# Kernel optimization log

Measured on AMD Instinct MI355X. Metric: run time of the kernel, lower is better.

## Reference

```python
import jax, jax.numpy as jnp
import numpy as np

C0, C1 = 8, 4            # scalar / vector channels (type_in = type_out = [8,4])
K = 5                    # p-space kernel size
G = 8                    # number of gaussian radial basis functions
EPS = 1e-6               # zero-length epsilon
R_MAX = 5.5              # max |p_off - q_diff| ~ sqrt(3)*2 + 2


def _levi_civita():
    e = np.zeros((3, 3, 3), np.float32)
    e[0, 1, 2] = e[1, 2, 0] = e[2, 0, 1] = 1.0
    e[0, 2, 1] = e[2, 1, 0] = e[1, 0, 2] = -1.0
    return jnp.asarray(e)


def setup_inputs() -> dict:
    key = jax.random.key(0)
    ks = jax.random.split(key, 10)
    N, Q, P = 1, 16, 8
    dim = C0 + 3 * C1
    x = jax.random.normal(ks[0], (N, dim, Q, P, P, P), jnp.float32)

    def qschema(k):
        q = jax.random.normal(k, (Q, 3), jnp.float32)
        return q / jnp.max(jnp.linalg.norm(q, axis=-1))  # normalize lengths to <= 1

    q_in, q_out = qschema(ks[1]), qschema(ks[2])
    s = 0.1
    w_ss = s * jax.random.normal(ks[3], (C0, C0, G), jnp.float32)
    w_vs = s * jax.random.normal(ks[4], (C1, C0, G), jnp.float32)
    w_sv = s * jax.random.normal(ks[5], (C0, C1, G), jnp.float32)
    w_vv0 = s * jax.random.normal(ks[6], (C1, C1, G), jnp.float32)
    w_vv1 = s * jax.random.normal(ks[7], (C1, C1, G), jnp.float32)
    bias = s * jax.random.normal(ks[8], (C0,), jnp.float32)
    return dict(x=x, q_in=q_in, q_out=q_out, w_ss=w_ss, w_vs=w_vs, w_sv=w_sv,
                w_vv0=w_vv0, w_vv1=w_vv1, bias=bias)


def reference(x, q_in, q_out, w_ss, w_vs, w_sv, w_vv0, w_vv1, bias):
    N, dim_in, Qi = x.shape[0], x.shape[1], x.shape[2]
    Qo = q_out.shape[0]
    K3 = K ** 3
    # p-space tap offsets (voxel units, zyx) of the 5x5x5 kernel
    offs = jnp.arange(K, dtype=x.dtype) - (K - 1) / 2.0
    oz, oy, ox = jnp.meshgrid(offs, offs, offs, indexing='ij')
    p_off = jnp.stack([oz, oy, ox], -1).reshape(-1, 3)                       # (K3,3)
    # pq_diff geometry: v = p_offset - (q_out - q_in)
    v = p_off[None, None] - (q_out[:, None, None] - q_in[None, :, None])     # (Qo,Qi,K3,3)
    r = jnp.linalg.norm(v, axis=-1)                                          # (Qo,Qi,K3)
    u = jnp.where(r[..., None] > EPS, v / jnp.maximum(r, EPS)[..., None], 0.0)
    # gaussian radial basis on |v|
    centers = jnp.linspace(0.0, R_MAX, G).astype(x.dtype)
    sigma = R_MAX / (G - 1)
    R = jnp.exp(-0.5 * ((r[..., None] - centers) / sigma) ** 2)              # (Qo,Qi,K3,G)
    RY = R[..., None] * u[..., None, :]                                      # (Qo,Qi,K3,G,3) radial x Y_1
    eye3 = jnp.eye(3, dtype=x.dtype)
    eps3 = _levi_civita().astype(x.dtype)
    # CG paths (l_in,l_out,l_f): axes a=out ch, c=in ch, p=Qo, q=Qi, k=tap, g=radial, m/n/i/j=vec comps
    K_ss = jnp.einsum('acg,pqkg->apcqk', w_ss, R)                            # (0,0,0)
    K_vs = jnp.einsum('acg,pqkgm->ampcqk', w_vs, RY)                         # (0,1,1)
    K_sv = jnp.einsum('acg,pqkgm->apcmqk', w_sv, RY)                         # (1,0,1)
    K_vv = (jnp.einsum('acg,pqkg,mn->ampcnqk', w_vv0, R, eye3)               # (1,1,0) identity
            + 0.7071067811865476 *
            jnp.einsum('acg,pqkgm,imj->aipcjqk', w_vv1, RY, eps3))           # (1,1,1) cross prod
    top = jnp.concatenate([K_ss, K_sv.reshape(C0, Qo, 3 * C1, Qi, K3)], axis=2)
    bot = jnp.concatenate([K_vs.reshape(3 * C1, Qo, C0, Qi, K3),
                           K_vv.reshape(3 * C1, Qo, 3 * C1, Qi, K3)], axis=2)
    kern = jnp.concatenate([top, bot], axis=0)                               # (dim_out,Qo,dim_in,Qi,K3)
    dim_out = C0 + 3 * C1
    kern = kern.reshape(dim_out * Qo, dim_in * Qi, K, K, K)
    xr = x.reshape(N, dim_in * Qi, *x.shape[3:])
    out = jax.lax.conv_general_dilated(
        xr, kern, window_strides=(1, 1, 1), padding='SAME',
        dimension_numbers=('NCDHW', 'OIDHW', 'NCDHW'))
    out = out.reshape(N, dim_out, Qo, *x.shape[3:])
    b_full = jnp.concatenate([bias, jnp.zeros(3 * C1, bias.dtype)])
    return out + b_full.reshape(1, dim_out, 1, 1, 1, 1)
```

## Files before the change

kernel.cpp:

```cpp
#include <hip/hip_runtime.h>
#include <hip/hip_bf16.h>
#include <math.h>

#define C0 8
#define C1 4
#define NCH 20
#define NQ 16
#define K3 125
#define G 8
#define RMAX 5.5f
#define EPSL 1e-6f

#define KD1 2048
#define PHI_N 1048576
#define XTP_N 552960
#define W2_N 20480
#define KD2 640
#define E2C_B 10485760

#define LDS_A 18432
#define LDS_B 27648

using f32x4 = __attribute__((ext_vector_type(4))) float;
using s16x8 = __attribute__((ext_vector_type(8))) short;

__device__ __forceinline__ float epsf(int i, int m, int j) {
    if (i == m || m == j || i == j) return 0.f;
    return (m == (i + 1) % 3) ? 1.f : -1.f;
}

__global__ __launch_bounds__(256) void prep_kernel(
    const float* __restrict__ x,
    const float* __restrict__ q_in, const float* __restrict__ q_out,
    const float* __restrict__ w_ss, const float* __restrict__ w_vs,
    const float* __restrict__ w_sv, const float* __restrict__ w_vv0,
    const float* __restrict__ w_vv1,
    __hip_bfloat16* __restrict__ phi, __hip_bfloat16* __restrict__ xtp,
    __hip_bfloat16* __restrict__ w2)
{
    int gid = blockIdx.x * 256 + threadIdx.x;
    if (gid < PHI_N) {
        int col = gid & (KD1 - 1); int m = gid >> 11;
        int t = col >> 4, q = col & 15;
        int p = m >> 5,  b = m & 31;
        int g = b >> 2,  mi = b & 3;
        float val = 0.f;
        if (t < K3) {
            int tz = t / 25, ty = (t / 5) % 5, tx = t % 5;
            float vz = (float)(tz - 2) - (q_out[p*3+0] - q_in[q*3+0]);
            float vy = (float)(ty - 2) - (q_out[p*3+1] - q_in[q*3+1]);
            float vx = (float)(tx - 2) - (q_out[p*3+2] - q_in[q*3+2]);
            float r  = sqrtf(vz*vz + vy*vy + vx*vx);
            float inv = (r > EPSL) ? (1.0f / r) : 0.0f;
            const float sigma = RMAX / (float)(G - 1);
            float d = (r - (RMAX * (float)g / (float)(G - 1))) / sigma;
            float Rg = expf(-0.5f * d * d);
            float u = (mi == 1) ? vz*inv : ((mi == 2) ? vy*inv : vx*inv);
            val = (mi == 0) ? Rg : Rg * u;
        }
        phi[gid] = __float2bfloat16(val);
    } else if (gid < PHI_N + XTP_N) {
        int g2 = gid - PHI_N;
        int q = g2 & 15; int r = g2 >> 4;
        int ax = r % 12; r /= 12;
        int ay = r % 12; r /= 12;
        int az = r % 12; int c = r / 12;
        int iz = az - 2, iy = ay - 2, ix = ax - 2;
        bool valid = ((unsigned)iz < 8u) & ((unsigned)iy < 8u) & ((unsigned)ix < 8u);
        float v = valid ? x[((c * NQ + q) << 9) + (iz << 6) + (iy << 3) + ix] : 0.f;
        xtp[g2] = __float2bfloat16(v);
    } else {
        int id = gid - (PHI_N + XTP_N);
        int b = id & 31; int r = id >> 5;
        int c = r % NCH; int o = r / NCH;
        int g = b >> 2,  mi = b & 3;
        float val = 0.f;
        if (o < NCH) {
            if (o < C0) {
                if (c < C0) { if (mi == 0) val = w_ss[(o * C0 + c) * G + g]; }
                else { int cv = (c - C0) / 3, j = (c - C0) % 3;
                       if (mi == 1 + j) val = w_sv[(o * C1 + cv) * G + g]; }
            } else {
                int ov = (o - C0) / 3, i = (o - C0) % 3;
                if (c < C0) { if (mi == 1 + i) val = w_vs[(ov * C0 + c) * G + g]; }
                else {
                    int cv = (c - C0) / 3, j = (c - C0) % 3;
                    if (mi == 0) { if (i == j) val = w_vv0[(ov * C1 + cv) * G + g]; }
                    else val = 0.7071067811865476f * w_vv1[(ov * C1 + cv) * G + g]
                               * epsf(i, mi - 1, j);
                }
            }
        }
        w2[id] = __float2bfloat16(val);
    }
}

__global__ __launch_bounds__(256, 3) void gemm1_kernel(
    const char* __restrict__ phi_b, const char* __restrict__ xtp_b,
    char* __restrict__ E2_b)
{
    __shared__ __align__(16) char lds[LDS_A + LDS_B];

    int tid = threadIdx.x;
    int wave = tid >> 6, lane = tid & 63;
    int row = lane & 15, quad = lane >> 4;
    int wi = wave >> 1, wj = wave & 1;

    int bi = blockIdx.x;
    int kc = bi / 320;
    int r  = bi - kc * 320;
    int pg = r / 80;
    int r2 = r - pg * 80;
    int c  = r2 >> 2;
    int zq = r2 & 3;

    {
        const char* src = xtp_b + c * 55296 + zq * 9216;
        for (int i = tid; i < 1728; i += 256)
            *(s16x8*)(lds + LDS_A + i * 16) = *(const s16x8*)(src + i * 16);
    }

    const char* abase = phi_b + (size_t)(pg * 128) * 4096 + kc * 2048;
    int srow[4], skp[4];
    #pragma unroll
    for (int i = 0; i < 4; ++i) { int s = tid + i * 256; srow[i] = s >> 3; skp[i] = s & 7; }
    s16x8 areg[4];
    #pragma unroll
    for (int i = 0; i < 4; ++i)
        areg[i] = *(const s16x8*)(abase + srow[i] * 4096 + skp[i] * 16);

    int bpre[4];
    #pragma unroll
    for (int nt = 0; nt < 4; ++nt) {
        int zl = wj * 64 + nt * 16 + row;
        int zz = zl >> 6, zy = (zl >> 3) & 7, zx = zl & 7;
        bpre[nt] = LDS_A + (zz * 144 + zy * 12 + zx) * 32 + (quad & 1) * 16;
    }
    int hi = quad >> 1;

    f32x4 acc[4][4];
    #pragma unroll
    for (int i = 0; i < 4; ++i)
        #pragma unroll
        for (int j = 0; j < 4; ++j) acc[i][j] = (f32x4){0.f, 0.f, 0.f, 0.f};

    for (int j = 0; j < 16; ++j) {
        int toff[4];
        #pragma unroll
        for (int tt = 0; tt < 4; ++tt) {
            int t = kc * 64 + j * 4 + tt; if (t > 124) t = 124;
            int tz = t / 25, trm = t - tz * 25;
            int ty = trm / 5, tx = trm - ty * 5;
            toff[tt] = (tz * 144 + ty * 12 + tx) * 32;
        }
        #pragma unroll
        for (int i = 0; i < 4; ++i)
            *(s16x8*)(lds + srow[i] * 144 + skp[i] * 16) = areg[i];
        __syncthreads();
        if (j < 15) {
            #pragma unroll
            for (int i = 0; i < 4; ++i)
                areg[i] = *(const s16x8*)(abase + srow[i] * 4096 + (j + 1) * 128 + skp[i] * 16);
        }
        #pragma unroll
        for (int st = 0; st < 2; ++st) {
            s16x8 af[4], bf[4];
            #pragma unroll
            for (int mt = 0; mt < 4; ++mt)
                af[mt] = *(const s16x8*)(lds + (wi * 64 + mt * 16 + row) * 144
                                             + (st * 4 + quad) * 16);
            int tsel = toff[st * 2 + hi];
            #pragma unroll
            for (int nt = 0; nt < 4; ++nt)
                bf[nt] = *(const s16x8*)(lds + bpre[nt] + tsel);
            #pragma unroll
            for (int mt = 0; mt < 4; ++mt)
                #pragma unroll
                for (int nt = 0; nt < 4; ++nt)
                    acc[mt][nt] = __builtin_amdgcn_mfma_f32_16x16x32_bf16(
                        af[mt], bf[nt], acc[mt][nt], 0, 0, 0);
        }
        __syncthreads();
    }

    int wbase = wave * 8704;
    #pragma unroll
    for (int mt = 0; mt < 4; ++mt) {
        #pragma unroll
        for (int nt = 0; nt < 4; ++nt) {
            int zl = nt * 16 + row;
            union { unsigned long long u; __hip_bfloat16 h[4]; } pk;
            pk.h[0] = __float2bfloat16(acc[mt][nt][0]);
            pk.h[1] = __float2bfloat16(acc[mt][nt][1]);
            pk.h[2] = __float2bfloat16(acc[mt][nt][2]);
            pk.h[3] = __float2bfloat16(acc[mt][nt][3]);
            *(unsigned long long*)(lds + wbase + zl * 136 + (mt * 16 + quad * 4) * 2) = pk.u;
        }
    }
    char* Ek = E2_b + (size_t)kc * E2C_B;
    int pbase = pg * 4 + wi * 2;
    #pragma unroll
    for (int it = 0; it < 8; ++it) {
        int item = lane + it * 64;
        int piece = item & 3;
        int zl = (item >> 2) & 63;
        int h  = item >> 8;
        s16x8 v = *(const s16x8*)(lds + wbase + zl * 136 + h * 64 + piece * 16);
        int p = pbase + h;
        int z = zq * 128 + wj * 64 + zl;
        *(s16x8*)(Ek + ((size_t)((p * NCH + c) << 9) + z) * 64 + piece * 16) = v;
    }
}

__global__ __launch_bounds__(128) void gemm2_kernel(
    const char* __restrict__ w2_b, const char* __restrict__ E2_b,
    const float* __restrict__ bias, float* __restrict__ out)
{
    int tid = threadIdx.x;
    int wave = tid >> 6, lane = tid & 63;
    int row = lane & 15, quad = lane >> 4;
    int bi = blockIdx.x;
    int p  = bi >> 4;
    int zb = bi & 15;
    int z  = zb * 32 + wave * 16 + row;

    const char* bbase = E2_b + (size_t)p * 655360 + (size_t)z * 64 + quad * 16;

    f32x4 acc[2];
    acc[0] = (f32x4){0.f, 0.f, 0.f, 0.f};
    acc[1] = (f32x4){0.f, 0.f, 0.f, 0.f};

    for (int kc = 0; kc < 2; ++kc) {
        const char* bk = bbase + (size_t)kc * E2C_B;
        #pragma unroll 5
        for (int cc = 0; cc < NCH; ++cc) {
            s16x8 a0 = *(const s16x8*)(w2_b + (row)      * 1280 + cc * 64 + quad * 16);
            s16x8 a1 = *(const s16x8*)(w2_b + (16 + row) * 1280 + cc * 64 + quad * 16);
            s16x8 b  = *(const s16x8*)(bk + (size_t)cc * 32768);
            acc[0] = __builtin_amdgcn_mfma_f32_16x16x32_bf16(a0, b, acc[0], 0, 0, 0);
            acc[1] = __builtin_amdgcn_mfma_f32_16x16x32_bf16(a1, b, acc[1], 0, 0, 0);
        }
    }

    #pragma unroll
    for (int mt = 0; mt < 2; ++mt)
        #pragma unroll
        for (int ri = 0; ri < 4; ++ri) {
            int o = mt * 16 + quad * 4 + ri;
            if (o < NCH)
                out[((o * NQ + p) << 9) + z] = acc[mt][ri] + ((o < C0) ? bias[o] : 0.f);
        }
}

extern "C" void kernel_launch(void* const* d_in, const int* in_sizes, int n_in,
                              void* d_out, int out_size, void* d_ws, size_t ws_size,
                              hipStream_t stream) {
    const float* x     = (const float*)d_in[0];
    const float* q_in  = (const float*)d_in[1];
    const float* q_out = (const float*)d_in[2];
    const float* w_ss  = (const float*)d_in[3];
    const float* w_vs  = (const float*)d_in[4];
    const float* w_sv  = (const float*)d_in[5];
    const float* w_vv0 = (const float*)d_in[6];
    const float* w_vv1 = (const float*)d_in[7];
    const float* bias  = (const float*)d_in[8];
    float* out = (float*)d_out;

    char* ws = (char*)d_ws;
    __hip_bfloat16* phi = (__hip_bfloat16*)(ws + 0);
    __hip_bfloat16* xtp = (__hip_bfloat16*)(ws + 2097152);
    __hip_bfloat16* w2  = (__hip_bfloat16*)(ws + 3203072);
    char*           E2  = (char*)(ws + 3244032);

    const int PREP_N = PHI_N + XTP_N + W2_N;
    hipLaunchKernelGGL(prep_kernel, dim3(PREP_N / 256), dim3(256), 0, stream,
                       x, q_in, q_out, w_ss, w_vs, w_sv, w_vv0, w_vv1, phi, xtp, w2);
    hipLaunchKernelGGL(gemm1_kernel, dim3(640), dim3(256), 0, stream,
                       (const char*)phi, (const char*)xtp, E2);
    hipLaunchKernelGGL(gemm2_kernel, dim3(256), dim3(128), 0, stream,
                       (const char*)w2, (const char*)E2, bias, out);
}
```

Measured before the change: 117.3 us.

## Split gemm2 reduction across blocks with atomic accumulation and bias prefill

Splits the gemm2 reduction over the two kc chunks and two channel halves into separate blocks, growing the grid from 256 to 1024 blocks to occupy more CUs. Partial sums are combined with float atomicAdd into the output. The output is first filled with the bias (or zero) by an extra section of prep_kernel. This adds atomic traffic, makes the summation order nondeterministic, and adds an output initialization pass.

```diff
diff --git a/kernel.cpp b/kernel.cpp
--- a/kernel.cpp
+++ b/kernel.cpp
@@ -15,7 +15,7 @@
 #define PHI_N 1048576
 #define XTP_N 552960
 #define W2_N 20480
-#define KD2 640
+#define OUT_N 163840
 #define E2C_B 10485760
 
 #define LDS_A 18432
@@ -34,9 +34,9 @@
     const float* __restrict__ q_in, const float* __restrict__ q_out,
     const float* __restrict__ w_ss, const float* __restrict__ w_vs,
     const float* __restrict__ w_sv, const float* __restrict__ w_vv0,
-    const float* __restrict__ w_vv1,
+    const float* __restrict__ w_vv1, const float* __restrict__ bias,
     __hip_bfloat16* __restrict__ phi, __hip_bfloat16* __restrict__ xtp,
-    __hip_bfloat16* __restrict__ w2)
+    __hip_bfloat16* __restrict__ w2, float* __restrict__ out)
 {
     int gid = blockIdx.x * 256 + threadIdx.x;
     if (gid < PHI_N) {
@@ -69,7 +69,7 @@
         bool valid = ((unsigned)iz < 8u) & ((unsigned)iy < 8u) & ((unsigned)ix < 8u);
         float v = valid ? x[((c * NQ + q) << 9) + (iz << 6) + (iy << 3) + ix] : 0.f;
         xtp[g2] = __float2bfloat16(v);
-    } else {
+    } else if (gid < PHI_N + XTP_N + W2_N) {
         int id = gid - (PHI_N + XTP_N);
         int b = id & 31; int r = id >> 5;
         int c = r % NCH; int o = r / NCH;
@@ -92,6 +92,10 @@
             }
         }
         w2[id] = __float2bfloat16(val);
+    } else {
+        int id = gid - (PHI_N + XTP_N + W2_N);
+        int o = id >> 13;
+        out[id] = (o < C0) ? bias[o] : 0.f;
     }
 }
 
@@ -214,32 +218,33 @@
 
 __global__ __launch_bounds__(128) void gemm2_kernel(
     const char* __restrict__ w2_b, const char* __restrict__ E2_b,
-    const float* __restrict__ bias, float* __restrict__ out)
+    float* __restrict__ out)
 {
     int tid = threadIdx.x;
     int wave = tid >> 6, lane = tid & 63;
     int row = lane & 15, quad = lane >> 4;
     int bi = blockIdx.x;
-    int p  = bi >> 4;
-    int zb = bi & 15;
+    int p  = bi >> 6;
+    int zb = (bi >> 2) & 15;
+    int kc = (bi >> 1) & 1;
+    int ch = bi & 1;
     int z  = zb * 32 + wave * 16 + row;
 
-    const char* bbase = E2_b + (size_t)p * 655360 + (size_t)z * 64 + quad * 16;
+    const char* bbase = E2_b + (size_t)kc * E2C_B + (size_t)p * 655360
+                        + (size_t)z * 64 + quad * 16;
 
     f32x4 acc[2];
     acc[0] = (f32x4){0.f, 0.f, 0.f, 0.f};
     acc[1] = (f32x4){0.f, 0.f, 0.f, 0.f};
 
-    for (int kc = 0; kc < 2; ++kc) {
-        const char* bk = bbase + (size_t)kc * E2C_B;
-        #pragma unroll 5
-        for (int cc = 0; cc < NCH; ++cc) {
-            s16x8 a0 = *(const s16x8*)(w2_b + (row)      * 1280 + cc * 64 + quad * 16);
-            s16x8 a1 = *(const s16x8*)(w2_b + (16 + row) * 1280 + cc * 64 + quad * 16);
-            s16x8 b  = *(const s16x8*)(bk + (size_t)cc * 32768);
-            acc[0] = __builtin_amdgcn_mfma_f32_16x16x32_bf16(a0, b, acc[0], 0, 0, 0);
-            acc[1] = __builtin_amdgcn_mfma_f32_16x16x32_bf16(a1, b, acc[1], 0, 0, 0);
-        }
+    #pragma unroll 5
+    for (int ci = 0; ci < 10; ++ci) {
+        int cc = ch * 10 + ci;
+        s16x8 a0 = *(const s16x8*)(w2_b + (row)      * 1280 + cc * 64 + quad * 16);
+        s16x8 a1 = *(const s16x8*)(w2_b + (16 + row) * 1280 + cc * 64 + quad * 16);
+        s16x8 b  = *(const s16x8*)(bbase + (size_t)cc * 32768);
+        acc[0] = __builtin_amdgcn_mfma_f32_16x16x32_bf16(a0, b, acc[0], 0, 0, 0);
+        acc[1] = __builtin_amdgcn_mfma_f32_16x16x32_bf16(a1, b, acc[1], 0, 0, 0);
     }
 
     #pragma unroll
@@ -248,7 +253,7 @@
         for (int ri = 0; ri < 4; ++ri) {
             int o = mt * 16 + quad * 4 + ri;
             if (o < NCH)
-                out[((o * NQ + p) << 9) + z] = acc[mt][ri] + ((o < C0) ? bias[o] : 0.f);
+                atomicAdd(out + ((o * NQ + p) << 9) + z, acc[mt][ri]);
         }
 }
 
@@ -272,11 +277,12 @@
     __hip_bfloat16* w2  = (__hip_bfloat16*)(ws + 3203072);
     char*           E2  = (char*)(ws + 3244032);
 
-    const int PREP_N = PHI_N + XTP_N + W2_N;
+    const int PREP_N = PHI_N + XTP_N + W2_N + OUT_N;
     hipLaunchKernelGGL(prep_kernel, dim3(PREP_N / 256), dim3(256), 0, stream,
-                       x, q_in, q_out, w_ss, w_vs, w_sv, w_vv0, w_vv1, phi, xtp, w2);
+                       x, q_in, q_out, w_ss, w_vs, w_sv, w_vv0, w_vv1, bias,
+                       phi, xtp, w2, out);
     hipLaunchKernelGGL(gemm1_kernel, dim3(640), dim3(256), 0, stream,
                        (const char*)phi, (const char*)xtp, E2);
-    hipLaunchKernelGGL(gemm2_kernel, dim3(256), dim3(128), 0, stream,
-                       (const char*)w2, (const char*)E2, bias, out);
-}
+    hipLaunchKernelGGL(gemm2_kernel, dim3(1024), dim3(128), 0, stream,
+                       (const char*)w2, (const char*)E2, out);
+}
```

Result: faster. 114.3 us (-2.6%).
